# Kernel tuning notes

Hardware: AMD Instinct MI355X
Metric: run time of the kernel (lower is better)

The kernel has to match this reference:

```python
import jax, jax.numpy as jnp
import numpy as np

N_TRIPLES = 100_000    # number of (head, rel, attr) triples
TOTAL_CHARS = 1_600_000  # total characters across all attribute strings (~16/triple)
CHAR_VOCAB = 10_000
N_ENT = 100_000
D = 128                # embedding dim shared by char and entity tables


def setup_inputs() -> dict:
    key = jax.random.key(0)
    k1, k2, k3, k4, k5 = jax.random.split(key, 5)
    char_embeddings = jax.random.normal(k1, (CHAR_VOCAB, D), dtype=jnp.float32)
    entity_embeddings = jax.random.normal(k2, (N_ENT, D), dtype=jnp.float32)
    head_ids = jax.random.randint(k3, (N_TRIPLES,), 0, N_ENT, dtype=jnp.int32)
    char_ids = jax.random.randint(k4, (TOTAL_CHARS,), 0, CHAR_VOCAB, dtype=jnp.int32)
    # sorted segment ids emulate the per-triple ragged grouping (offsets form)
    segment_ids = jnp.sort(jax.random.randint(k5, (TOTAL_CHARS,), 0, N_TRIPLES, dtype=jnp.int32))
    return {
        "char_embeddings": char_embeddings,
        "entity_embeddings": entity_embeddings,
        "head_ids": head_ids,
        "char_ids": char_ids,
        "segment_ids": segment_ids,
    }


def reference(char_embeddings, entity_embeddings, head_ids, char_ids, segment_ids):
    n = head_ids.shape[0]
    # ragged embedding-bag: gather char rows, sum within each triple's segment
    t = jax.ops.segment_sum(char_embeddings[char_ids], segment_ids, num_segments=n)  # [N, D]
    h = entity_embeddings[head_ids]  # [N, D]
    # torch.norm with no dim = global Frobenius norm (faithful to original)
    h = h / jnp.linalg.norm(h)
    t = t / jnp.linalg.norm(t)
    return jnp.sum(1.0 - jnp.sum(h * t, axis=1))
```

## Files before the change

kernel.cpp:

```cpp
#include <hip/hip_runtime.h>

#define DIM   128
#define HALF  64
#define CPT   256
#define TAIL  64
#define WPB   4
#define QD    24

__global__ __launch_bounds__(256) void fused_kernel(
    const float* __restrict__ char_emb,
    const float* __restrict__ ent,
    const int* __restrict__ head_ids,
    const int* __restrict__ char_ids,
    const int* __restrict__ seg_ids,
    float* __restrict__ pb,
    int total_chars, int n_triples)
{
    __shared__ __align__(16) int s_off[WPB][CPT + TAIL];
    __shared__ int s_sid[WPB][CPT + TAIL];
    __shared__ __align__(16) int s_hq[WPB][QD];
    __shared__ float s_hv[WPB][QD][64];
    __shared__ float r_scr[3][WPB];

    const int tid  = threadIdx.x;
    const int lane = tid & 63;
    const int wid  = tid >> 6;
    const int colb = lane << 2;

    float ht = 0.f, tt = 0.f, hh = 0.f;

    const int slice = blockIdx.x & 1;
    const int sco   = slice << 8;
    const int chunk = (blockIdx.x >> 1) * WPB + wid;
    const int start = chunk * CPT;
    const int len   = min(CPT, total_chars - start);
    const int sl    = min(CPT + TAIL, total_chars - start);
    const char* cb  = (const char*)char_emb;
    const float* ee = ent + slice * HALF + lane;

    for (int c = lane; c < sl; c += 64) {
        s_off[wid][c] = (char_ids[start + c] << 9) + sco;
        s_sid[wid][c] = seg_ids[start + c];
    }

    unsigned long long mk[4] = {0ull, 0ull, 0ull, 0ull};
    int nbq = 0;
    if (len == CPT) {
        int rbase = 0;
#pragma unroll
        for (int grp = 0; grp < 4; ++grp) {
            const int c = start + grp * 64 + lane;
            const int s1 = seg_ids[c];
            const int s0 = (c > 0) ? seg_ids[c - 1] : (s1 + 1);
            const bool bnd = (s1 != s0);
            mk[grp] = __ballot(bnd);
            const int rk = rbase + (int)__popcll(mk[grp] & ((1ull << lane) - 1ull));
            if (bnd && rk < QD) s_hq[wid][rk] = head_ids[s1];
            rbase += (int)__popcll(mk[grp]);
        }
        nbq = min(rbase, QD);

        int r = 0;
        for (; r + 4 <= nbq; r += 4) {
            const int4 q4 = *(const int4*)&s_hq[wid][r];
            const int h0 = __builtin_amdgcn_readfirstlane(q4.x);
            const int h1 = __builtin_amdgcn_readfirstlane(q4.y);
            const int h2 = __builtin_amdgcn_readfirstlane(q4.z);
            const int h3 = __builtin_amdgcn_readfirstlane(q4.w);
            const float v0 = ee[(size_t)h0 * DIM];
            const float v1 = ee[(size_t)h1 * DIM];
            const float v2 = ee[(size_t)h2 * DIM];
            const float v3 = ee[(size_t)h3 * DIM];
            hh = fmaf(v0, v0, hh); hh = fmaf(v1, v1, hh);
            hh = fmaf(v2, v2, hh); hh = fmaf(v3, v3, hh);
            s_hv[wid][r + 0][lane] = v0;
            s_hv[wid][r + 1][lane] = v1;
            s_hv[wid][r + 2][lane] = v2;
            s_hv[wid][r + 3][lane] = v3;
        }
        for (; r < nbq; ++r) {
            const int h0 = __builtin_amdgcn_readfirstlane(s_hq[wid][r]);
            const float v0 = ee[(size_t)h0 * DIM];
            hh = fmaf(v0, v0, hh);
            s_hv[wid][r][lane] = v0;
        }
    }
    __syncthreads();

    if (len == CPT) {
        int cur = (start > 0) ? seg_ids[start - 1]
                              : __builtin_amdgcn_readfirstlane(s_sid[wid][0]);
        float hv = 0.f;
        float pv = s_hv[wid][0][lane];
        float acc = 0.f;
        bool live = false;
        int rk = 0;
        float vA[16], vB[16];

#define PF(BUF, B) { \
    _Pragma("unroll") \
    for (int q = 0; q < 4; ++q) { \
        const int4 o4 = *(const int4*)&s_off[wid][(B) * 16 + q * 4]; \
        BUF[q * 4 + 0] = *(const float*)(cb + (size_t)(unsigned)(o4.x + colb)); \
        BUF[q * 4 + 1] = *(const float*)(cb + (size_t)(unsigned)(o4.y + colb)); \
        BUF[q * 4 + 2] = *(const float*)(cb + (size_t)(unsigned)(o4.z + colb)); \
        BUF[q * 4 + 3] = *(const float*)(cb + (size_t)(unsigned)(o4.w + colb)); \
    } }

#define CS(BUF, B) { \
    _Pragma("unroll") \
    for (int j = 0; j < 16; ++j) { \
        if (mk[(B) >> 2] & (1ull << (((B) & 3) * 16 + j))) {    \
            if (live) { ht = fmaf(hv, acc, ht); tt = fmaf(acc, acc, tt); } \
            live = true; \
            acc = 0.f; \
            const int news = __builtin_amdgcn_readfirstlane(s_sid[wid][(B) * 16 + j]); \
            if (news > cur + 1) {                \
                for (int g = cur + 1; g < news; ++g) { \
                    const float gv = ee[(size_t)head_ids[g] * DIM]; \
                    hh = fmaf(gv, gv, hh); \
                } \
            } \
            cur = news; \
            if (rk < QD) {                       \
                hv = pv; \
                const int nxt = (rk + 1 < QD) ? rk + 1 : QD - 1; \
                pv = s_hv[wid][nxt][lane]; \
            } else {                             \
                hv = ee[(size_t)head_ids[cur] * DIM]; \
                hh = fmaf(hv, hv, hh); \
            } \
            ++rk; \
        } \
        acc += BUF[j]; \
    } }

        PF(vA, 0)
#pragma unroll
        for (int B = 0; B < 16; ++B) {
            if (B + 1 < 16) { if (B & 1) { PF(vA, B + 1) } else { PF(vB, B + 1) } }
            if (B & 1) { CS(vB, B) } else { CS(vA, B) }
        }

        if (live) {
            int e = CPT;
            bool ended = false;
            while (e < sl) {
                const int idx = e + lane;
                const bool differ = (idx < sl) && (s_sid[wid][idx] != cur);
                const unsigned long long bm = __ballot(differ);
                const int run = bm ? (__ffsll((long long)bm) - 1)
                                   : min(64, sl - e);
                for (int j = 0; j < run; j += 4) {
                    const int mm2 = min(4, run - j);
                    float vv[4];
#pragma unroll
                    for (int k = 0; k < 4; ++k) {
                        if (k < mm2)
                            vv[k] = *(const float*)(cb +
                                (size_t)(unsigned)(s_off[wid][e + j + k] + colb));
                    }
                    for (int k = 0; k < mm2; ++k) acc += vv[k];
                }
                e += run;
                if (bm) { ended = true; break; }
            }
            if (!ended && start + sl < total_chars) {
                int gg = start + sl;
                while (gg < total_chars && seg_ids[gg] == cur) {
                    acc += *(const float*)(cb +
                        (size_t)(unsigned)((char_ids[gg] << 9) + sco + colb));
                    ++gg;
                }
            }
            ht = fmaf(hv, acc, ht);
            tt = fmaf(acc, acc, tt);
        }
    } else if (len > 0) {
        const float* cembF = char_emb + slice * HALF + lane;
        int p = 0;
        if (start > 0) {
            const int prev = seg_ids[start - 1];
            while (p < len && seg_ids[start + p] == prev) ++p;
        }
        if (p < len) {
            int cur2 = seg_ids[start + p];
            if (start > 0) {
                for (int g = seg_ids[start - 1] + 1; g < cur2; ++g) {
                    const float gv = ee[(size_t)head_ids[g] * DIM];
                    hh = fmaf(gv, gv, hh);
                }
            }
            float acc = 0.f;
            float hv = ee[(size_t)head_ids[cur2] * DIM];
            hh = fmaf(hv, hv, hh);
            for (int c = p; c < len; ++c) {
                const int sid = seg_ids[start + c];
                if (sid != cur2) {
                    ht += hv * acc; tt += acc * acc;
                    for (int g = cur2 + 1; g < sid; ++g) {
                        const float gv = ee[(size_t)head_ids[g] * DIM];
                        hh = fmaf(gv, gv, hh);
                    }
                    acc = 0.f; cur2 = sid;
                    hv = ee[(size_t)head_ids[cur2] * DIM];
                    hh = fmaf(hv, hv, hh);
                }
                acc += cembF[(size_t)char_ids[start + c] * DIM];
            }
            int gg = start + len;
            while (gg < total_chars && seg_ids[gg] == cur2) {
                acc += cembF[(size_t)char_ids[gg] * DIM];
                ++gg;
            }
            ht += hv * acc; tt += acc * acc;
        }
    }

#pragma unroll
    for (int off = 32; off > 0; off >>= 1) {
        ht += __shfl_down(ht, off);
        tt += __shfl_down(tt, off);
        hh += __shfl_down(hh, off);
    }
    if (lane == 0) { r_scr[0][wid] = ht; r_scr[1][wid] = tt; r_scr[2][wid] = hh; }
    __syncthreads();
    if (tid == 0) {
        float a = 0.f, b = 0.f, c = 0.f;
#pragma unroll
        for (int w = 0; w < WPB; ++w) {
            a += r_scr[0][w]; b += r_scr[1][w]; c += r_scr[2][w];
        }
        pb[blockIdx.x * 3 + 0] = a;
        pb[blockIdx.x * 3 + 1] = b;
        pb[blockIdx.x * 3 + 2] = c;
    }
}

__global__ __launch_bounds__(256) void reduce_kernel(
    const float* __restrict__ pb, int nb, float* __restrict__ out,
    int n_triples, const int* __restrict__ seg_ids,
    const int* __restrict__ head_ids, const float* __restrict__ ent,
    int total_chars)
{
    double ht = 0.0, tt = 0.0, hh = 0.0;
    for (int i = threadIdx.x; i < nb; i += 256) {
        ht += (double)pb[i * 3 + 0];
        tt += (double)pb[i * 3 + 1];
        hh += (double)pb[i * 3 + 2];
    }
    int first = n_triples, last = n_triples - 1;
    if (total_chars > 0) { first = seg_ids[0]; last = seg_ids[total_chars - 1]; }
    const int lead  = first;
    const int trail = n_triples - 1 - last;
    const int tot   = lead + trail;
    const float4* e4 = (const float4*)ent;
    for (int w = threadIdx.x; w < tot * 32; w += 256) {
        const int rr = w >> 5;
        const int g  = (rr < lead) ? rr : (last + 1 + (rr - lead));
        const float4 v = e4[(size_t)head_ids[g] * 32 + (w & 31)];
        hh += (double)v.x * v.x + (double)v.y * v.y
            + (double)v.z * v.z + (double)v.w * v.w;
    }
#pragma unroll
    for (int off = 32; off > 0; off >>= 1) {
        ht += __shfl_down(ht, off);
        tt += __shfl_down(tt, off);
        hh += __shfl_down(hh, off);
    }
    __shared__ double sd[3][4];
    const int wid = threadIdx.x >> 6;
    if ((threadIdx.x & 63) == 0) { sd[0][wid] = ht; sd[1][wid] = tt; sd[2][wid] = hh; }
    __syncthreads();
    if (threadIdx.x == 0) {
        double a = 0.0, b = 0.0, c = 0.0;
        for (int w = 0; w < 4; ++w) { a += sd[0][w]; b += sd[1][w]; c += sd[2][w]; }
        out[0] = (float)((double)n_triples - a / sqrt(c * b));
    }
}

extern "C" void kernel_launch(void* const* d_in, const int* in_sizes, int n_in,
                              void* d_out, int out_size, void* d_ws, size_t ws_size,
                              hipStream_t stream)
{
    const float* char_emb = (const float*)d_in[0];
    const float* ent_emb  = (const float*)d_in[1];
    const int* head_ids   = (const int*)d_in[2];
    const int* char_ids   = (const int*)d_in[3];
    const int* seg_ids    = (const int*)d_in[4];
    const int n_triples   = in_sizes[2];
    const int total_chars = in_sizes[3];

    const int n_chunks = (total_chars + CPT - 1) / CPT;
    const int bps = (n_chunks + WPB - 1) / WPB;
    const int nsb = (2 * bps > 0) ? 2 * bps : 2;

    float* pb = (float*)d_ws;

    fused_kernel<<<nsb, 256, 0, stream>>>(char_emb, ent_emb, head_ids,
                                          char_ids, seg_ids, pb,
                                          total_chars, n_triples);
    reduce_kernel<<<1, 256, 0, stream>>>(pb, nsb, (float*)d_out, n_triples,
                                         seg_ids, head_ids, ent_emb,
                                         total_chars);
}
```

Baseline: 186.7 us.

## Replace shared-memory head staging with a register prefetch queue; hoist gap handling

Stops preloading every head-entity row into shared memory behind a block-wide barrier. Each wave now keeps a 4-deep register ring of upcoming head rows, loaded as segment boundaries are consumed, so the entity gathers overlap the char-embedding accumulation. Heads of empty segments (gaps) are now summed into the norm during the boundary-detection pass instead of inside the hot loop. The queue depth grows from 24 to 32. In exchange the entity loads are issued closer to where they are used, which may expose latency, and the gap loop now runs serially per gap lane.

```diff
diff --git a/kernel.cpp b/kernel.cpp
--- a/kernel.cpp
+++ b/kernel.cpp
@@ -5,7 +5,7 @@
 #define CPT   256
 #define TAIL  64
 #define WPB   4
-#define QD    24
+#define QD    32
 
 __global__ __launch_bounds__(256) void fused_kernel(
     const float* __restrict__ char_emb,
@@ -18,8 +18,7 @@
 {
     __shared__ __align__(16) int s_off[WPB][CPT + TAIL];
     __shared__ int s_sid[WPB][CPT + TAIL];
-    __shared__ __align__(16) int s_hq[WPB][QD];
-    __shared__ float s_hv[WPB][QD][64];
+    __shared__ int s_hq[WPB][QD];
     __shared__ float r_scr[3][WPB];
 
     const int tid  = threadIdx.x;
@@ -54,47 +53,34 @@
             const int s0 = (c > 0) ? seg_ids[c - 1] : (s1 + 1);
             const bool bnd = (s1 != s0);
             mk[grp] = __ballot(bnd);
-            const int rk = rbase + (int)__popcll(mk[grp] & ((1ull << lane) - 1ull));
-            if (bnd && rk < QD) s_hq[wid][rk] = head_ids[s1];
+            const int rk0 = rbase + (int)__popcll(mk[grp] & ((1ull << lane) - 1ull));
+            if (bnd && rk0 < QD) s_hq[wid][rk0] = head_ids[s1];
             rbase += (int)__popcll(mk[grp]);
+            unsigned long long gapm = __ballot(s1 > s0 + 1);
+            while (gapm) {
+                const int l  = __ffsll((long long)gapm) - 1;
+                const int g0 = __shfl(s0, l);
+                const int g1 = __shfl(s1, l);
+                for (int g = g0 + 1; g < g1; ++g) {
+                    const float gv = ee[(size_t)head_ids[g] * DIM];
+                    hh = fmaf(gv, gv, hh);
+                }
+                gapm &= gapm - 1;
+            }
         }
         nbq = min(rbase, QD);
-
-        int r = 0;
-        for (; r + 4 <= nbq; r += 4) {
-            const int4 q4 = *(const int4*)&s_hq[wid][r];
-            const int h0 = __builtin_amdgcn_readfirstlane(q4.x);
-            const int h1 = __builtin_amdgcn_readfirstlane(q4.y);
-            const int h2 = __builtin_amdgcn_readfirstlane(q4.z);
-            const int h3 = __builtin_amdgcn_readfirstlane(q4.w);
-            const float v0 = ee[(size_t)h0 * DIM];
-            const float v1 = ee[(size_t)h1 * DIM];
-            const float v2 = ee[(size_t)h2 * DIM];
-            const float v3 = ee[(size_t)h3 * DIM];
-            hh = fmaf(v0, v0, hh); hh = fmaf(v1, v1, hh);
-            hh = fmaf(v2, v2, hh); hh = fmaf(v3, v3, hh);
-            s_hv[wid][r + 0][lane] = v0;
-            s_hv[wid][r + 1][lane] = v1;
-            s_hv[wid][r + 2][lane] = v2;
-            s_hv[wid][r + 3][lane] = v3;
-        }
-        for (; r < nbq; ++r) {
-            const int h0 = __builtin_amdgcn_readfirstlane(s_hq[wid][r]);
-            const float v0 = ee[(size_t)h0 * DIM];
-            hh = fmaf(v0, v0, hh);
-            s_hv[wid][r][lane] = v0;
-        }
-    }
-    __syncthreads();
+    }
 
     if (len == CPT) {
-        int cur = (start > 0) ? seg_ids[start - 1]
-                              : __builtin_amdgcn_readfirstlane(s_sid[wid][0]);
         float hv = 0.f;
-        float pv = s_hv[wid][0][lane];
         float acc = 0.f;
         bool live = false;
         int rk = 0;
+        float r0 = 0.f, r1 = 0.f, r2 = 0.f, r3 = 0.f;
+        if (nbq > 0) r0 = ee[(size_t)__builtin_amdgcn_readfirstlane(s_hq[wid][0]) * DIM];
+        if (nbq > 1) r1 = ee[(size_t)__builtin_amdgcn_readfirstlane(s_hq[wid][1]) * DIM];
+        if (nbq > 2) r2 = ee[(size_t)__builtin_amdgcn_readfirstlane(s_hq[wid][2]) * DIM];
+        if (nbq > 3) r3 = ee[(size_t)__builtin_amdgcn_readfirstlane(s_hq[wid][3]) * DIM];
         float vA[16], vB[16];
 
 #define PF(BUF, B) { \
@@ -114,22 +100,17 @@
             if (live) { ht = fmaf(hv, acc, ht); tt = fmaf(acc, acc, tt); } \
             live = true; \
             acc = 0.f; \
-            const int news = __builtin_amdgcn_readfirstlane(s_sid[wid][(B) * 16 + j]); \
-            if (news > cur + 1) {                \
-                for (int g = cur + 1; g < news; ++g) { \
-                    const float gv = ee[(size_t)head_ids[g] * DIM]; \
-                    hh = fmaf(gv, gv, hh); \
-                } \
+            if (rk < QD) {                       \
+                hv = r0; r0 = r1; r1 = r2; r2 = r3; \
+                const int ni = rk + 4; \
+                r3 = (ni < nbq) \
+                   ? ee[(size_t)__builtin_amdgcn_readfirstlane(s_hq[wid][ni]) * DIM] \
+                   : 0.f; \
+            } else {                             \
+                const int cs = __builtin_amdgcn_readfirstlane(s_sid[wid][(B) * 16 + j]); \
+                hv = ee[(size_t)head_ids[cs] * DIM]; \
             } \
-            cur = news; \
-            if (rk < QD) {                       \
-                hv = pv; \
-                const int nxt = (rk + 1 < QD) ? rk + 1 : QD - 1; \
-                pv = s_hv[wid][nxt][lane]; \
-            } else {                             \
-                hv = ee[(size_t)head_ids[cur] * DIM]; \
-                hh = fmaf(hv, hv, hh); \
-            } \
+            hh = fmaf(hv, hv, hh);               \
             ++rk; \
         } \
         acc += BUF[j]; \
@@ -143,6 +124,7 @@
         }
 
         if (live) {
+            int cur = __builtin_amdgcn_readfirstlane(s_sid[wid][CPT - 1]);
             int e = CPT;
             bool ended = false;
             while (e < sl) {
```

Result: faster. 178.5 us (-4.4%).
